# Performance work log

Measured on AMD Instinct MI355X. Metric: run time of the kernel, lower is better.

## Reference

```python
import jax, jax.numpy as jnp
import numpy as np

B, C, H, W = 64, 3, 384, 384
P = 16                      # patch_size
E = 768                     # embed_dim
NH, NW = H // P, W // P     # 24, 24
N = NH * NW                 # 576 patches


def setup_inputs() -> dict:
    key = jax.random.key(0)
    k_x, k_y, k_xs, k_w, k_b = jax.random.split(key, 5)
    x = jax.random.normal(k_x, (B, C, H, W), dtype=jnp.float32)
    ys = jax.random.randint(k_y, (B, N), 0, W - P, dtype=jnp.int32)
    xs = jax.random.randint(k_xs, (B, N), 0, W - P, dtype=jnp.int32)
    # Conv2d(in_chans, embed_dim, kernel=P, stride=P) parameters
    w = jax.random.normal(k_w, (E, C, P, P), dtype=jnp.float32) * 0.02
    b = jax.random.normal(k_b, (E,), dtype=jnp.float32) * 0.02
    return {"x": x, "ys": ys, "xs": xs, "w": w, "b": b}


def _gather_patches(x, ys, xs):
    # x: [B,C,H,W]; ys/xs: [B,N] top-left corners -> patches [B,N,C,P,P]
    def one_img(img, ys_b, xs_b):
        def one_patch(y, x0):
            return jax.lax.dynamic_slice(img, (0, y, x0), (C, P, P))
        return jax.vmap(one_patch)(ys_b, xs_b)
    return jax.vmap(one_img)(x, ys, xs)


def reference(x, ys, xs, w, b):
    # patch_positions, as in the torch module
    patch_positions = jnp.stack([ys, xs], axis=-1)          # [B,N,2]
    patches = _gather_patches(x, ys, xs)                    # [B,N,C,P,P]
    # Restitched image fed to a stride-P conv == per-patch projection.
    # Conv windows exactly coincide with the restitched patches, so the
    # patch_embed is a single contraction per patch (same math, one pass).
    tokens = jnp.einsum('bncpq,ecpq->bne', patches, w) + b  # [B,N,E]
    return tokens, patch_positions
```

## Files before the change

### kernel.cpp

```cpp
#include <hip/hip_runtime.h>

#define B_    64
#define C_    3
#define H_    384
#define W_    384
#define P_    16
#define E_    768
#define N_    576
#define M_    (B_ * N_)
#define K_    (C_ * P_ * P_)

#define BM    128
#define BN    128
#define BK    64

typedef __attribute__((ext_vector_type(8))) short  short8;
typedef __attribute__((ext_vector_type(4))) float  f32x4;

__device__ __forceinline__ unsigned short f2bf(float f) {
    unsigned int u = __float_as_uint(f);
    u += 0x7FFFu + ((u >> 16) & 1u);
    return (unsigned short)(u >> 16);
}

__device__ __forceinline__ void gload_lds16(const void* g, void* l) {
    __builtin_amdgcn_global_load_lds(
        (const __attribute__((address_space(1))) unsigned int*)g,
        (__attribute__((address_space(3))) unsigned int*)l,
        16, 0, 0);
}

__global__ __launch_bounds__(256)
void gather_kernel(const float* __restrict__ x,
                   const int*   __restrict__ ys,
                   const int*   __restrict__ xs,
                   unsigned short* __restrict__ Abf)
{
    const unsigned g = blockIdx.x * 256 + threadIdx.x;
    const unsigned patch = g / 192u;
    const unsigned r  = g - patch * 192u;
    const unsigned c  = r >> 6;
    const unsigned r2 = r & 63u;
    const unsigned py = r2 >> 2;
    const unsigned q  = r2 & 3u;

    const unsigned bimg = patch / (unsigned)N_;
    const int y  = ys[patch];
    const int xx = xs[patch];

    const float* src = x + (size_t)bimg * (C_ * H_ * W_)
                         + (size_t)c * (H_ * W_)
                         + (size_t)(y + py) * W_ + xx + q * 4;

    uint2 pk;
    pk.x = (unsigned)f2bf(src[0]) | ((unsigned)f2bf(src[1]) << 16);
    pk.y = (unsigned)f2bf(src[2]) | ((unsigned)f2bf(src[3]) << 16);
    *(uint2*)(Abf + (size_t)g * 4) = pk;
}

__global__ __launch_bounds__(256)
void wconv_kernel(const float* __restrict__ w, unsigned short* __restrict__ Wb)
{
    const unsigned g = blockIdx.x * 256 + threadIdx.x;
    float4 f = ((const float4*)w)[g];
    uint2 pk;
    pk.x = (unsigned)f2bf(f.x) | ((unsigned)f2bf(f.y) << 16);
    pk.y = (unsigned)f2bf(f.z) | ((unsigned)f2bf(f.w) << 16);
    *(uint2*)(Wb + (size_t)g * 4) = pk;
}

__global__ __launch_bounds__(256)
void gemm_bf16(const unsigned short* __restrict__ A,
               const unsigned short* __restrict__ Wb,
               const float* __restrict__ bias,
               float*       __restrict__ out)
{
    __shared__ unsigned short Asm[BM * BK];
    __shared__ unsigned short Bsm[BN * BK];

    const int t    = threadIdx.x;
    const int wave = t >> 6;
    const int lane = t & 63;

    const int b   = blockIdx.x;
    const int xcd = b & 7;
    const int idx = b >> 3;
    const int mt  = xcd * 36 + idx / 6;
    const int et  = idx % 6;
    const int m0  = mt * BM;
    const int e0  = et * BN;

    const int r8 = lane >> 3;
    const int c8 = (lane & 7) * 8;
    const unsigned short* Ag = A  + (size_t)(m0 + wave * 32 + r8) * K_ + c8;
    const unsigned short* Bg = Wb + (size_t)(e0 + wave * 32 + r8) * K_ + c8;
    unsigned short* Al = &Asm[(wave * 32 + r8) * BK + c8];
    unsigned short* Bl = &Bsm[(wave * 32 + r8) * BK + c8];

    const int wr   = (wave >> 1) * 64;
    const int wc   = (wave & 1) * 64;
    const int lm   = lane & 15;
    const int quad = lane >> 4;

    f32x4 acc[4][4];
#pragma unroll
    for (int i = 0; i < 4; ++i)
#pragma unroll
        for (int j = 0; j < 4; ++j)
            acc[i][j] = (f32x4){0.f, 0.f, 0.f, 0.f};

#pragma unroll 1
    for (int it = 0; it < K_ / BK; ++it) {
        const unsigned short* ag = Ag + it * BK;
        const unsigned short* bg = Bg + it * BK;
#pragma unroll
        for (int inst = 0; inst < 4; ++inst) {
            gload_lds16(ag + (size_t)(inst * 8) * K_, Al + inst * 8 * BK);
            gload_lds16(bg + (size_t)(inst * 8) * K_, Bl + inst * 8 * BK);
        }

        __syncthreads();

#pragma unroll
        for (int s = 0; s < 2; ++s) {
            short8 af[4], bfr[4];
#pragma unroll
            for (int i = 0; i < 4; ++i)
                af[i] = *(const short8*)&Asm[(wr + i * 16 + lm) * BK + s * 32 + quad * 8];
#pragma unroll
            for (int j = 0; j < 4; ++j)
                bfr[j] = *(const short8*)&Bsm[(wc + j * 16 + lm) * BK + s * 32 + quad * 8];
#pragma unroll
            for (int i = 0; i < 4; ++i)
#pragma unroll
                for (int j = 0; j < 4; ++j)
                    acc[i][j] = __builtin_amdgcn_mfma_f32_16x16x32_bf16(af[i], bfr[j], acc[i][j], 0, 0, 0);
        }

        __syncthreads();
    }

    float bv[4];
#pragma unroll
    for (int j = 0; j < 4; ++j) bv[j] = bias[e0 + wc + j * 16 + lm];

#pragma unroll
    for (int i = 0; i < 4; ++i) {
#pragma unroll
        for (int j = 0; j < 4; ++j) {
            const int eo = e0 + wc + j * 16 + lm;
#pragma unroll
            for (int r = 0; r < 4; ++r) {
                const int mo = m0 + wr + i * 16 + quad * 4 + r;
                out[(size_t)mo * E_ + eo] = acc[i][j][r] + bv[j];
            }
        }
    }
}

__global__ void pos_kernel(const int* __restrict__ ys, const int* __restrict__ xs,
                           float* __restrict__ outp)
{
    int i = blockIdx.x * blockDim.x + threadIdx.x;
    if (i < M_) {
        outp[2 * i]     = (float)ys[i];
        outp[2 * i + 1] = (float)xs[i];
    }
}

extern "C" void kernel_launch(void* const* d_in, const int* in_sizes, int n_in,
                              void* d_out, int out_size, void* d_ws, size_t ws_size,
                              hipStream_t stream)
{
    const float* x    = (const float*)d_in[0];
    const int*   ys   = (const int*)d_in[1];
    const int*   xs   = (const int*)d_in[2];
    const float* w    = (const float*)d_in[3];
    const float* bias = (const float*)d_in[4];
    float* out = (float*)d_out;

    unsigned short* Abf = (unsigned short*)d_ws;
    unsigned short* Wb  = Abf + (size_t)M_ * K_;

    gather_kernel<<<(M_ * 192) / 256, 256, 0, stream>>>(x, ys, xs, Abf);
    wconv_kernel<<<(E_ * K_ / 4) / 256, 256, 0, stream>>>(w, Wb);

    gemm_bf16<<<(M_ / BM) * (E_ / BN), 256, 0, stream>>>(Abf, Wb, bias, out);

    float* outp = out + (size_t)M_ * E_;
    pos_kernel<<<(M_ + 255) / 256, 256, 0, stream>>>(ys, xs, outp);
}
```

Before: 270.7 us.

## Fuse patch gather and bf16 conversion into GEMM A-tile loading

Removes the separate gather kernel and its bf16 workspace. The GEMM now reads raw fp32 patch rows directly from the image, converts them to bf16 in registers, and writes them into LDS with an XOR swizzle. The next K-slice is prefetched into registers while the MFMAs run. This saves a full write and re-read of the im2col matrix. In exchange, each of the 6 column-tile blocks re-gathers the same patches from the image, and register pressure goes up.

```diff
diff --git a/kernel.cpp b/kernel.cpp
--- a/kernel.cpp
+++ b/kernel.cpp
@@ -9,18 +9,28 @@
 #define N_    576
 #define M_    (B_ * N_)
 #define K_    (C_ * P_ * P_)
+#define HW_   (H_ * W_)
+#define CHW_  (C_ * H_ * W_)
 
 #define BM    128
 #define BN    128
 #define BK    64
+#define KITERS (K_ / BK)
 
 typedef __attribute__((ext_vector_type(8))) short  short8;
 typedef __attribute__((ext_vector_type(4))) float  f32x4;
 
-__device__ __forceinline__ unsigned short f2bf(float f) {
-    unsigned int u = __float_as_uint(f);
-    u += 0x7FFFu + ((u >> 16) & 1u);
-    return (unsigned short)(u >> 16);
+__device__ __forceinline__ unsigned int rnepair(float a, float b) {
+    unsigned ua = __float_as_uint(a), ub = __float_as_uint(b);
+    ua += 0x7FFFu + ((ua >> 16) & 1u);
+    ub += 0x7FFFu + ((ub >> 16) & 1u);
+    return (ua >> 16) | (ub & 0xFFFF0000u);
+}
+
+__device__ __forceinline__ float4 ld16u(const float* p) {
+    float4 v;
+    __builtin_memcpy(&v, p, 16);
+    return v;
 }
 
 __device__ __forceinline__ void gload_lds16(const void* g, void* l) {
@@ -31,52 +41,26 @@
 }
 
 __global__ __launch_bounds__(256)
-void gather_kernel(const float* __restrict__ x,
-                   const int*   __restrict__ ys,
-                   const int*   __restrict__ xs,
-                   unsigned short* __restrict__ Abf)
-{
-    const unsigned g = blockIdx.x * 256 + threadIdx.x;
-    const unsigned patch = g / 192u;
-    const unsigned r  = g - patch * 192u;
-    const unsigned c  = r >> 6;
-    const unsigned r2 = r & 63u;
-    const unsigned py = r2 >> 2;
-    const unsigned q  = r2 & 3u;
-
-    const unsigned bimg = patch / (unsigned)N_;
-    const int y  = ys[patch];
-    const int xx = xs[patch];
-
-    const float* src = x + (size_t)bimg * (C_ * H_ * W_)
-                         + (size_t)c * (H_ * W_)
-                         + (size_t)(y + py) * W_ + xx + q * 4;
-
-    uint2 pk;
-    pk.x = (unsigned)f2bf(src[0]) | ((unsigned)f2bf(src[1]) << 16);
-    pk.y = (unsigned)f2bf(src[2]) | ((unsigned)f2bf(src[3]) << 16);
-    *(uint2*)(Abf + (size_t)g * 4) = pk;
-}
-
-__global__ __launch_bounds__(256)
 void wconv_kernel(const float* __restrict__ w, unsigned short* __restrict__ Wb)
 {
     const unsigned g = blockIdx.x * 256 + threadIdx.x;
     float4 f = ((const float4*)w)[g];
     uint2 pk;
-    pk.x = (unsigned)f2bf(f.x) | ((unsigned)f2bf(f.y) << 16);
-    pk.y = (unsigned)f2bf(f.z) | ((unsigned)f2bf(f.w) << 16);
+    pk.x = rnepair(f.x, f.y);
+    pk.y = rnepair(f.z, f.w);
     *(uint2*)(Wb + (size_t)g * 4) = pk;
 }
 
 __global__ __launch_bounds__(256)
-void gemm_bf16(const unsigned short* __restrict__ A,
-               const unsigned short* __restrict__ Wb,
-               const float* __restrict__ bias,
-               float*       __restrict__ out)
-{
-    __shared__ unsigned short Asm[BM * BK];
-    __shared__ unsigned short Bsm[BN * BK];
+void fused_gemm(const float* __restrict__ x,
+                const int*   __restrict__ ys,
+                const int*   __restrict__ xs,
+                const unsigned short* __restrict__ Wb,
+                const float* __restrict__ bias,
+                float*       __restrict__ out)
+{
+    __shared__ __align__(16) unsigned short Asm[BM * BK];
+    __shared__ __align__(16) unsigned short Bsm[BN * BK];
 
     const int t    = threadIdx.x;
     const int wave = t >> 6;
@@ -90,17 +74,28 @@
     const int m0  = mt * BM;
     const int e0  = et * BN;
 
+    const int p  = t >> 1;
+    const int h  = t & 1;
+    const int gp = m0 + p;
+    const int bimg  = gp / N_;
+    const int pbase = bimg * CHW_ + ys[gp] * W_ + xs[gp];
+    const float* xrow = x + pbase + 2 * h * W_;
+
+    char* aw = (char*)Asm + p * 128;
+    const int awz = (p & 7) << 4;
+    const int h64 = h * 64;
+
     const int r8 = lane >> 3;
     const int c8 = (lane & 7) * 8;
-    const unsigned short* Ag = A  + (size_t)(m0 + wave * 32 + r8) * K_ + c8;
     const unsigned short* Bg = Wb + (size_t)(e0 + wave * 32 + r8) * K_ + c8;
-    unsigned short* Al = &Asm[(wave * 32 + r8) * BK + c8];
     unsigned short* Bl = &Bsm[(wave * 32 + r8) * BK + c8];
 
     const int wr   = (wave >> 1) * 64;
     const int wc   = (wave & 1) * 64;
     const int lm   = lane & 15;
     const int quad = lane >> 4;
+    const char* Ard = (const char*)Asm + (wr + lm) * 128;
+    const int rswz = (lm & 7) << 4;
 
     f32x4 acc[4][4];
 #pragma unroll
@@ -109,24 +104,47 @@
         for (int j = 0; j < 4; ++j)
             acc[i][j] = (f32x4){0.f, 0.f, 0.f, 0.f};
 
+    float4 fr[8];
+#pragma unroll
+    for (int m = 0; m < 4; ++m) fr[m]     = ld16u(xrow + 4 * m);
+#pragma unroll
+    for (int m = 0; m < 4; ++m) fr[4 + m] = ld16u(xrow + W_ + 4 * m);
+
 #pragma unroll 1
-    for (int it = 0; it < K_ / BK; ++it) {
-        const unsigned short* ag = Ag + it * BK;
+    for (int it = 0; it < KITERS; ++it) {
         const unsigned short* bg = Bg + it * BK;
 #pragma unroll
-        for (int inst = 0; inst < 4; ++inst) {
-            gload_lds16(ag + (size_t)(inst * 8) * K_, Al + inst * 8 * BK);
+        for (int inst = 0; inst < 4; ++inst)
             gload_lds16(bg + (size_t)(inst * 8) * K_, Bl + inst * 8 * BK);
+
+#pragma unroll
+        for (int j = 0; j < 4; ++j) {
+            uint4 wv;
+            wv.x = rnepair(fr[2*j].x,   fr[2*j].y);
+            wv.y = rnepair(fr[2*j].z,   fr[2*j].w);
+            wv.z = rnepair(fr[2*j+1].x, fr[2*j+1].y);
+            wv.w = rnepair(fr[2*j+1].z, fr[2*j+1].w);
+            *(uint4*)(aw + ((h64 + j * 16) ^ awz)) = wv;
         }
 
         __syncthreads();
+
+        if (it + 1 < KITERS) {
+            const int itn = it + 1;
+            const float* rp = xrow + (itn >> 2) * HW_ + ((itn & 3) << 2) * W_;
+#pragma unroll
+            for (int m = 0; m < 4; ++m) fr[m]     = ld16u(rp + 4 * m);
+#pragma unroll
+            for (int m = 0; m < 4; ++m) fr[4 + m] = ld16u(rp + W_ + 4 * m);
+        }
 
 #pragma unroll
         for (int s = 0; s < 2; ++s) {
             short8 af[4], bfr[4];
 #pragma unroll
             for (int i = 0; i < 4; ++i)
-                af[i] = *(const short8*)&Asm[(wr + i * 16 + lm) * BK + s * 32 + quad * 8];
+                af[i] = *(const short8*)(Ard + i * (16 * 128)
+                                             + ((s * 64 + quad * 16) ^ rswz));
 #pragma unroll
             for (int j = 0; j < 4; ++j)
                 bfr[j] = *(const short8*)&Bsm[(wc + j * 16 + lm) * BK + s * 32 + quad * 8];
@@ -179,13 +197,11 @@
     const float* bias = (const float*)d_in[4];
     float* out = (float*)d_out;
 
-    unsigned short* Abf = (unsigned short*)d_ws;
-    unsigned short* Wb  = Abf + (size_t)M_ * K_;
-
-    gather_kernel<<<(M_ * 192) / 256, 256, 0, stream>>>(x, ys, xs, Abf);
+    unsigned short* Wb = (unsigned short*)d_ws;
+
     wconv_kernel<<<(E_ * K_ / 4) / 256, 256, 0, stream>>>(w, Wb);
 
-    gemm_bf16<<<(M_ / BM) * (E_ / BN), 256, 0, stream>>>(Abf, Wb, bias, out);
+    fused_gemm<<<(M_ / BM) * (E_ / BN), 256, 0, stream>>>(x, ys, xs, Wb, bias, out);
 
     float* outp = out + (size_t)M_ * E_;
     pos_kernel<<<(M_ + 255) / 256, 256, 0, stream>>>(ys, xs, outp);
```

Measured after the change: 304.6 us. 12.5% more time.

## Double-buffer GEMM LDS tiles with prefetch and XOR-swizzled layout

Applied to the files above, without the earlier changes.

Converts the bf16 GEMM main loop to a two-stage LDS double buffer. Tile it+2 is prefetched through global_load_lds while tile it is consumed, with explicit vmcnt waits and s_barrier in place of __syncthreads. It also applies an XOR swizzle on the K offset, permuting the global source columns so the LDS layout is swizzled, and reads fragments with the matching XOR to cut LDS bank conflicts. The bias load is hoisted before the loop. LDS use doubles, which may reduce occupancy, and the hand-written waitcnt logic adds correctness risk.

```diff
diff --git a/kernel.cpp b/kernel.cpp
--- a/kernel.cpp
+++ b/kernel.cpp
@@ -13,6 +13,8 @@
 #define BM    128
 #define BN    128
 #define BK    64
+#define KITERS (K_ / BK)
+#define TILE_ELEMS (BM * BK)
 
 typedef __attribute__((ext_vector_type(8))) short  short8;
 typedef __attribute__((ext_vector_type(4))) float  f32x4;
@@ -75,8 +77,8 @@
                const float* __restrict__ bias,
                float*       __restrict__ out)
 {
-    __shared__ unsigned short Asm[BM * BK];
-    __shared__ unsigned short Bsm[BN * BK];
+    __shared__ __align__(16) unsigned short Asm[2][TILE_ELEMS];
+    __shared__ __align__(16) unsigned short Bsm[2][TILE_ELEMS];
 
     const int t    = threadIdx.x;
     const int wave = t >> 6;
@@ -92,15 +94,17 @@
 
     const int r8 = lane >> 3;
     const int c8 = (lane & 7) * 8;
-    const unsigned short* Ag = A  + (size_t)(m0 + wave * 32 + r8) * K_ + c8;
-    const unsigned short* Bg = Wb + (size_t)(e0 + wave * 32 + r8) * K_ + c8;
-    unsigned short* Al = &Asm[(wave * 32 + r8) * BK + c8];
-    unsigned short* Bl = &Bsm[(wave * 32 + r8) * BK + c8];
+    const int cx = c8 ^ (r8 << 3);
+    const unsigned short* Ag = A  + (size_t)(m0 + wave * 32 + r8) * K_ + cx;
+    const unsigned short* Bg = Wb + (size_t)(e0 + wave * 32 + r8) * K_ + cx;
+    unsigned short* Al = &Asm[0][(wave * 32 + r8) * BK + c8];
+    unsigned short* Bl = &Bsm[0][(wave * 32 + r8) * BK + c8];
 
     const int wr   = (wave >> 1) * 64;
     const int wc   = (wave & 1) * 64;
     const int lm   = lane & 15;
     const int quad = lane >> 4;
+    const int rsw  = (lm & 7) << 3;
 
     f32x4 acc[4][4];
 #pragma unroll
@@ -109,27 +113,45 @@
         for (int j = 0; j < 4; ++j)
             acc[i][j] = (f32x4){0.f, 0.f, 0.f, 0.f};
 
+    float bv[4];
+#pragma unroll
+    for (int j = 0; j < 4; ++j) bv[j] = bias[e0 + wc + j * 16 + lm];
+
+#define STAGE(tt, bsel)                                                       \
+    do {                                                                      \
+        const int _ko = (tt) * BK;                                            \
+        const int _lo = (bsel) * TILE_ELEMS;                                  \
+        _Pragma("unroll")                                                     \
+        for (int _i = 0; _i < 4; ++_i) {                                      \
+            gload_lds16(Ag + _ko + (size_t)(_i * 8) * K_, Al + _lo + _i * 8 * BK); \
+            gload_lds16(Bg + _ko + (size_t)(_i * 8) * K_, Bl + _lo + _i * 8 * BK); \
+        }                                                                     \
+    } while (0)
+
+    STAGE(0, 0);
+    STAGE(1, 1);
+
 #pragma unroll 1
-    for (int it = 0; it < K_ / BK; ++it) {
-        const unsigned short* ag = Ag + it * BK;
-        const unsigned short* bg = Bg + it * BK;
-#pragma unroll
-        for (int inst = 0; inst < 4; ++inst) {
-            gload_lds16(ag + (size_t)(inst * 8) * K_, Al + inst * 8 * BK);
-            gload_lds16(bg + (size_t)(inst * 8) * K_, Bl + inst * 8 * BK);
-        }
-
-        __syncthreads();
-
+    for (int it = 0; it < KITERS; ++it) {
+        if (it < KITERS - 1)
+            asm volatile("s_waitcnt vmcnt(8)" ::: "memory");
+        else
+            asm volatile("s_waitcnt vmcnt(0)" ::: "memory");
+        __builtin_amdgcn_sched_barrier(0);
+        __builtin_amdgcn_s_barrier();
+        __builtin_amdgcn_sched_barrier(0);
+
+        const int bo = (it & 1) * TILE_ELEMS;
 #pragma unroll
         for (int s = 0; s < 2; ++s) {
             short8 af[4], bfr[4];
+            const int eo2 = (s * 32 + quad * 8) ^ rsw;
 #pragma unroll
             for (int i = 0; i < 4; ++i)
-                af[i] = *(const short8*)&Asm[(wr + i * 16 + lm) * BK + s * 32 + quad * 8];
+                af[i]  = *(const short8*)&Asm[0][bo + (wr + i * 16 + lm) * BK + eo2];
 #pragma unroll
             for (int j = 0; j < 4; ++j)
-                bfr[j] = *(const short8*)&Bsm[(wc + j * 16 + lm) * BK + s * 32 + quad * 8];
+                bfr[j] = *(const short8*)&Bsm[0][bo + (wc + j * 16 + lm) * BK + eo2];
 #pragma unroll
             for (int i = 0; i < 4; ++i)
 #pragma unroll
@@ -137,12 +159,15 @@
                     acc[i][j] = __builtin_amdgcn_mfma_f32_16x16x32_bf16(af[i], bfr[j], acc[i][j], 0, 0, 0);
         }
 
-        __syncthreads();
+        asm volatile("s_waitcnt lgkmcnt(0)" ::: "memory");
+        __builtin_amdgcn_sched_barrier(0);
+        __builtin_amdgcn_s_barrier();
+        __builtin_amdgcn_sched_barrier(0);
+
+        if (it + 2 < KITERS)
+            STAGE(it + 2, it & 1);
     }
-
-    float bv[4];
-#pragma unroll
-    for (int j = 0; j < 4; ++j) bv[j] = bias[e0 + wc + j * 16 + lm];
+#undef STAGE
 
 #pragma unroll
     for (int i = 0; i < 4; ++i) {
```

New measurement: 285.4 us. 1.05x slower.
